# Kernel tuning notes

Hardware: AMD Instinct MI355X
Metric: run time of the kernel (lower is better)

## Reference

```python
import jax, jax.numpy as jnp
import numpy as np

LAMBDA_CONE = 0.5   # module-level constant in original repo
TAU_TEMP = 1.0      # softmax temperature
EPS = 1e-8


def setup_inputs() -> dict:
    key = jax.random.key(0)
    k1, k2, k3 = jax.random.split(key, 3)
    B, N, K, D = 8, 32768, 64, 64
    features = jax.random.normal(k1, (B, N, D), dtype=jnp.float32)
    slots = jax.random.normal(k2, (B, K, D), dtype=jnp.float32)
    horizons = jax.random.uniform(k3, (B, K), dtype=jnp.float32)  # positive horizons
    return {"features": features, "slots": slots, "horizons": horizons}


def _pairwise_minkowski(features, slots):
    # Minkowski split: channel 0 is time-like, channels 1: are space-like.
    ft, fs = features[..., 0], features[..., 1:]   # [B,N], [B,N,D-1]
    st, ss = slots[..., 0], slots[..., 1:]          # [B,K], [B,K,D-1]
    # dt[b,k,n] = t_feat - t_slot
    dt = ft[:, None, :] - st[:, :, None]            # [B,K,N]
    # squared spatial distance via the expansion ||f-s||^2 = ||f||^2 - 2 f.s + ||s||^2
    # (avoids materializing a [B,K,N,D] difference tensor)
    cross = jnp.einsum('bnd,bkd->bkn', fs, ss)      # [B,K,N]
    dx2 = (fs * fs).sum(-1)[:, None, :] - 2.0 * cross + (ss * ss).sum(-1)[:, :, None]
    dx2 = jnp.maximum(dx2, 0.0)                     # guard tiny negatives from expansion
    return dt, dx2


def reference(features, slots, horizons):
    dt, dx2 = _pairwise_minkowski(features, slots)  # [B,K,N] each
    # proper-time interval s^2 = dt^2 - |dx|^2; signed sqrt as the safe distance
    interval = dt * dt - dx2
    dist = jnp.sign(interval) * jnp.sqrt(jnp.abs(interval) + EPS)
    # cone score: how deep inside the light cone, scaled by per-slot horizon
    cone = (jnp.abs(dt) - jnp.sqrt(dx2 + EPS)) / (horizons[:, :, None] + EPS)
    logits = (-jnp.abs(dist) + jnp.tanh(cone) * LAMBDA_CONE) / TAU_TEMP
    attention = jax.nn.softmax(logits, axis=1)      # softmax over slots
    return attention
```

## Files before the change

kernel.cpp:

```cpp
#include <hip/hip_runtime.h>
#include <math.h>

#define EPSF 1e-8f

typedef _Float16 f16x8 __attribute__((ext_vector_type(8)));
typedef float    f32x4 __attribute__((ext_vector_type(4)));

constexpr int Bb = 8, Nn = 32768, Kk = 64, Dd = 64;

__global__ __launch_bounds__(256, 3) void attn_kernel(
    const float* __restrict__ features,
    const float* __restrict__ slots,
    const float* __restrict__ horizons,
    float* __restrict__ out)
{
    __shared__ float s_st[Kk], s_ss2[Kk], s_rh[Kk];

    const int tid  = threadIdx.x;
    const int bid  = blockIdx.x;
    const int b    = bid >> 7;
    const int blk  = bid & 127;
    const int lane = tid & 63;
    const int wid  = tid >> 6;
    const int m    = lane & 15;
    const int quad = lane >> 4;

    if (tid < Kk) {
        const float4* sr = (const float4*)(slots + (size_t)(b * Kk + tid) * Dd);
        float4 v = sr[0];
        float st = v.x;
        float ss = v.y * v.y + v.z * v.z + v.w * v.w;
        #pragma unroll
        for (int i = 1; i < 16; ++i) {
            float4 u = sr[i];
            ss += u.x * u.x + u.y * u.y + u.z * u.z + u.w * u.w;
        }
        s_st[tid]  = st;
        s_ss2[tid] = ss;
        s_rh[tid]  = 1.0f / (horizons[b * Kk + tid] + EPSF);
    }

    f16x8 a_hi[4][2], a_lo[4][2];
    #pragma unroll
    for (int t = 0; t < 4; ++t) {
        #pragma unroll
        for (int c = 0; c < 2; ++c) {
            const float* sp = slots + (size_t)(b * Kk + 16 * t + m) * Dd
                            + 32 * c + quad * 8;
            float4 u0 = *(const float4*)sp;
            float4 u1 = *(const float4*)(sp + 4);
            float fv[8] = {u0.x, u0.y, u0.z, u0.w, u1.x, u1.y, u1.z, u1.w};
            if (c == 0 && quad == 0) fv[0] = 0.0f;
            #pragma unroll
            for (int j = 0; j < 8; ++j) {
                float x = fv[j];
                _Float16 h = (_Float16)x;
                _Float16 l = (_Float16)(x - (float)h);
                a_hi[t][c][j] = h;
                a_lo[t][c][j] = l;
            }
        }
    }
    __syncthreads();

    #pragma unroll 1
    for (int it = 0; it < 4; ++it) {
        const int n0 = (blk * 16 + wid * 4 + it) * 16;

        f16x8 b_hi[2], b_lo[2];
        float f00 = 0.f, fs2p = 0.f;
        #pragma unroll
        for (int c = 0; c < 2; ++c) {
            const float* fp = features + (((size_t)b << 15) + n0 + m) * Dd
                            + 32 * c + quad * 8;
            float4 u0 = *(const float4*)fp;
            float4 u1 = *(const float4*)(fp + 4);
            float fv[8] = {u0.x, u0.y, u0.z, u0.w, u1.x, u1.y, u1.z, u1.w};
            if (c == 0) f00 = fv[0];
            #pragma unroll
            for (int j = 0; j < 8; ++j) {
                float x = fv[j];
                fs2p = fmaf(x, x, fs2p);
                _Float16 h = (_Float16)x;
                _Float16 l = (_Float16)(x - (float)h);
                b_hi[c][j] = h;
                b_lo[c][j] = l;
            }
        }
        const float ft = __shfl(f00, m);
        float fs2 = fs2p;
        fs2 += __shfl_xor(fs2, 16);
        fs2 += __shfl_xor(fs2, 32);
        fs2 = fmaf(-ft, ft, fs2);

        f32x4 acc[4];
        #pragma unroll
        for (int t = 0; t < 4; ++t) {
            f32x4 a = {0.f, 0.f, 0.f, 0.f};
            #pragma unroll
            for (int c = 0; c < 2; ++c) {
                a = __builtin_amdgcn_mfma_f32_16x16x32_f16(a_hi[t][c], b_hi[c], a, 0, 0, 0);
                a = __builtin_amdgcn_mfma_f32_16x16x32_f16(a_hi[t][c], b_lo[c], a, 0, 0, 0);
                a = __builtin_amdgcn_mfma_f32_16x16x32_f16(a_lo[t][c], b_hi[c], a, 0, 0, 0);
            }
            acc[t] = a;
        }

        float p[4][4];
        float sum = 0.f;
        #pragma unroll
        for (int t = 0; t < 4; ++t) {
            #pragma unroll
            for (int r = 0; r < 4; ++r) {
                const int k = 16 * t + quad * 4 + r;
                float st  = s_st[k];
                float ss2 = s_ss2[k];
                float rh  = s_rh[k];
                float cross = acc[t][r];
                float dt  = ft - st;
                float dx2 = fmaf(-2.f, cross, fs2 + ss2);
                dx2 = fmaxf(dx2, 0.f);
                float interval = fmaf(dt, dt, -dx2);
                float adist = __builtin_amdgcn_sqrtf(fabsf(interval) + EPSF);
                float cone  = (fabsf(dt) - __builtin_amdgcn_sqrtf(dx2 + EPSF)) * rh;
                float e  = __expf(2.0f * cone);
                float th = 1.0f - 2.0f * __builtin_amdgcn_rcpf(e + 1.0f);
                float logit = fmaf(0.5f, th, -adist);
                float pe = __expf(logit);
                p[t][r] = pe;
                sum += pe;
            }
        }
        sum += __shfl_xor(sum, 16);
        sum += __shfl_xor(sum, 32);
        const float inv = __builtin_amdgcn_rcpf(sum);

        float* ob = out + (((size_t)(b * Kk)) << 15) + n0 + m;
        #pragma unroll
        for (int t = 0; t < 4; ++t) {
            #pragma unroll
            for (int r = 0; r < 4; ++r) {
                const int k = 16 * t + quad * 4 + r;
                ob[(size_t)k << 15] = p[t][r] * inv;
            }
        }
    }
}

extern "C" void kernel_launch(void* const* d_in, const int* in_sizes, int n_in,
                              void* d_out, int out_size, void* d_ws, size_t ws_size,
                              hipStream_t stream) {
    const float* features = (const float*)d_in[0];
    const float* slots    = (const float*)d_in[1];
    const float* horizons = (const float*)d_in[2];
    float* out = (float*)d_out;

    hipLaunchKernelGGL(attn_kernel, dim3(1024), dim3(256), 0, stream,
                       features, slots, horizons, out);
}
```

Measured before the change: 144.8 us.

## Stage softmax outputs in LDS for float4 stores and prefetch next feature tile

Each wave now writes its unnormalized probabilities and per-column reciprocal sums into a padded LDS tile. Every two 16-column tiles it reads them back and emits 128-byte float4 row stores instead of scattered 64-byte scalar stores. Feature loads for the next tile are double-buffered in registers, and the launch bound hint goes from 3 to 4 blocks. This adds about 34KB of LDS per block and relies on 16-byte LDS reads at addresses whose row stride is padded to 33 floats, so some rows are not 16-byte aligned.

```diff
diff --git a/kernel.cpp b/kernel.cpp
--- a/kernel.cpp
+++ b/kernel.cpp
@@ -7,14 +7,17 @@
 typedef float    f32x4 __attribute__((ext_vector_type(4)));
 
 constexpr int Bb = 8, Nn = 32768, Kk = 64, Dd = 64;
+constexpr int PAD = 33;
 
-__global__ __launch_bounds__(256, 3) void attn_kernel(
+__global__ __launch_bounds__(256, 4) void attn_kernel(
     const float* __restrict__ features,
     const float* __restrict__ slots,
     const float* __restrict__ horizons,
     float* __restrict__ out)
 {
     __shared__ float s_st[Kk], s_ss2[Kk], s_rh[Kk];
+    __shared__ float s_p[4][Kk * PAD];
+    __shared__ float s_inv[4][32];
 
     const int tid  = threadIdx.x;
     const int bid  = blockIdx.x;
@@ -63,20 +66,39 @@
     }
     __syncthreads();
 
-    #pragma unroll 1
+    const int base_tile = blk * 16 + wid * 4;
+    float* const my_p   = s_p[wid];
+    float* const my_inv = s_inv[wid];
+
+    float4 buf[2][4];
+    {
+        const float* fp0 = features + (((size_t)b << 15) + (size_t)(base_tile) * 16 + m) * Dd
+                         + quad * 8;
+        buf[0][0] = *(const float4*)(fp0);
+        buf[0][1] = *(const float4*)(fp0 + 4);
+        buf[0][2] = *(const float4*)(fp0 + 32);
+        buf[0][3] = *(const float4*)(fp0 + 36);
+    }
+
+    #pragma unroll
     for (int it = 0; it < 4; ++it) {
-        const int n0 = (blk * 16 + wid * 4 + it) * 16;
+        if (it < 3) {
+            const float* fpn = features + (((size_t)b << 15) + (size_t)(base_tile + it + 1) * 16 + m) * Dd
+                             + quad * 8;
+            buf[(it + 1) & 1][0] = *(const float4*)(fpn);
+            buf[(it + 1) & 1][1] = *(const float4*)(fpn + 4);
+            buf[(it + 1) & 1][2] = *(const float4*)(fpn + 32);
+            buf[(it + 1) & 1][3] = *(const float4*)(fpn + 36);
+        }
 
         f16x8 b_hi[2], b_lo[2];
-        float f00 = 0.f, fs2p = 0.f;
+        const float f00 = buf[it & 1][0].x;
+        float fs2p = 0.f;
         #pragma unroll
         for (int c = 0; c < 2; ++c) {
-            const float* fp = features + (((size_t)b << 15) + n0 + m) * Dd
-                            + 32 * c + quad * 8;
-            float4 u0 = *(const float4*)fp;
-            float4 u1 = *(const float4*)(fp + 4);
+            float4 u0 = buf[it & 1][2 * c];
+            float4 u1 = buf[it & 1][2 * c + 1];
             float fv[8] = {u0.x, u0.y, u0.z, u0.w, u1.x, u1.y, u1.z, u1.w};
-            if (c == 0) f00 = fv[0];
             #pragma unroll
             for (int j = 0; j < 8; ++j) {
                 float x = fv[j];
@@ -106,7 +128,7 @@
             acc[t] = a;
         }
 
-        float p[4][4];
+        const int colb = (it & 1) * 16 + m;
         float sum = 0.f;
         #pragma unroll
         for (int t = 0; t < 4; ++t) {
@@ -127,22 +149,29 @@
                 float th = 1.0f - 2.0f * __builtin_amdgcn_rcpf(e + 1.0f);
                 float logit = fmaf(0.5f, th, -adist);
                 float pe = __expf(logit);
-                p[t][r] = pe;
+                my_p[k * PAD + colb] = pe;
                 sum += pe;
             }
         }
         sum += __shfl_xor(sum, 16);
         sum += __shfl_xor(sum, 32);
-        const float inv = __builtin_amdgcn_rcpf(sum);
+        my_inv[colb] = __builtin_amdgcn_rcpf(sum);
 
-        float* ob = out + (((size_t)(b * Kk)) << 15) + n0 + m;
-        #pragma unroll
-        for (int t = 0; t < 4; ++t) {
+        if (it & 1) {
+            asm volatile("s_waitcnt lgkmcnt(0)" ::: "memory");
+            const int r8 = lane >> 3;
+            const int c8 = lane & 7;
+            const size_t npair = (size_t)(base_tile + (it - 1)) * 16;
+            float4 iv = *(const float4*)(my_inv + c8 * 4);
+            float* ob = out + (((size_t)(b * Kk)) << 15) + npair + c8 * 4;
             #pragma unroll
-            for (int r = 0; r < 4; ++r) {
-                const int k = 16 * t + quad * 4 + r;
-                ob[(size_t)k << 15] = p[t][r] * inv;
+            for (int i = 0; i < 8; ++i) {
+                const int k = i * 8 + r8;
+                float4 v = *(const float4*)(my_p + k * PAD + c8 * 4);
+                v.x *= iv.x; v.y *= iv.y; v.z *= iv.z; v.w *= iv.w;
+                *(float4*)(ob + ((size_t)k << 15)) = v;
             }
+            asm volatile("s_waitcnt lgkmcnt(0)" ::: "memory");
         }
     }
 }
```

Result: slower. 170.9 us (+18.0%).

## Stage slot MFMA operands in LDS, prefetch features, double grid for occupancy

Applied to the files above, without the earlier changes.

The split-fp16 slot A-operands now live in shared memory. Each wave converts one 16-slot tile and all waves read them from LDS, where before every wave held all of them in registers. Register pressure drops, so launch bounds can rise to 4 blocks per CU. The grid doubles so each wave handles two 16-column tiles, with the second tile's feature loads issued before processing the first. The cost is extra LDS reads inside the MFMA loop and more blocks each redoing the slot preprocessing.

```diff
diff --git a/kernel.cpp b/kernel.cpp
--- a/kernel.cpp
+++ b/kernel.cpp
@@ -8,18 +8,20 @@
 
 constexpr int Bb = 8, Nn = 32768, Kk = 64, Dd = 64;
 
-__global__ __launch_bounds__(256, 3) void attn_kernel(
+__global__ __launch_bounds__(256, 4) void attn_kernel(
     const float* __restrict__ features,
     const float* __restrict__ slots,
     const float* __restrict__ horizons,
     float* __restrict__ out)
 {
     __shared__ float s_st[Kk], s_ss2[Kk], s_rh[Kk];
+    __shared__ f16x8 s_ahi[8][64];
+    __shared__ f16x8 s_alo[8][64];
 
     const int tid  = threadIdx.x;
     const int bid  = blockIdx.x;
-    const int b    = bid >> 7;
-    const int blk  = bid & 127;
+    const int b    = bid >> 8;
+    const int blk  = bid & 255;
     const int lane = tid & 63;
     const int wid  = tid >> 6;
     const int m    = lane & 15;
@@ -40,9 +42,8 @@
         s_rh[tid]  = 1.0f / (horizons[b * Kk + tid] + EPSF);
     }
 
-    f16x8 a_hi[4][2], a_lo[4][2];
-    #pragma unroll
-    for (int t = 0; t < 4; ++t) {
+    {
+        const int t = wid;
         #pragma unroll
         for (int c = 0; c < 2; ++c) {
             const float* sp = slots + (size_t)(b * Kk + 16 * t + m) * Dd
@@ -51,32 +52,53 @@
             float4 u1 = *(const float4*)(sp + 4);
             float fv[8] = {u0.x, u0.y, u0.z, u0.w, u1.x, u1.y, u1.z, u1.w};
             if (c == 0 && quad == 0) fv[0] = 0.0f;
+            f16x8 h8, l8;
             #pragma unroll
             for (int j = 0; j < 8; ++j) {
                 float x = fv[j];
                 _Float16 h = (_Float16)x;
                 _Float16 l = (_Float16)(x - (float)h);
-                a_hi[t][c][j] = h;
-                a_lo[t][c][j] = l;
+                h8[j] = h;
+                l8[j] = l;
             }
+            s_ahi[t * 2 + c][lane] = h8;
+            s_alo[t * 2 + c][lane] = l8;
         }
     }
     __syncthreads();
 
-    #pragma unroll 1
-    for (int it = 0; it < 4; ++it) {
-        const int n0 = (blk * 16 + wid * 4 + it) * 16;
+    const int base_tile = blk * 8 + wid * 2;
+
+    float4 buf[2][4];
+    {
+        const float* fp0 = features + (((size_t)b << 15) + (size_t)base_tile * 16 + m) * Dd
+                         + quad * 8;
+        buf[0][0] = *(const float4*)(fp0);
+        buf[0][1] = *(const float4*)(fp0 + 4);
+        buf[0][2] = *(const float4*)(fp0 + 32);
+        buf[0][3] = *(const float4*)(fp0 + 36);
+    }
+
+    #pragma unroll
+    for (int it = 0; it < 2; ++it) {
+        if (it == 0) {
+            const float* fpn = features + (((size_t)b << 15) + (size_t)(base_tile + 1) * 16 + m) * Dd
+                             + quad * 8;
+            buf[1][0] = *(const float4*)(fpn);
+            buf[1][1] = *(const float4*)(fpn + 4);
+            buf[1][2] = *(const float4*)(fpn + 32);
+            buf[1][3] = *(const float4*)(fpn + 36);
+        }
+        const int n0 = (base_tile + it) * 16;
 
         f16x8 b_hi[2], b_lo[2];
-        float f00 = 0.f, fs2p = 0.f;
+        const float f00 = buf[it][0].x;
+        float fs2p = 0.f;
         #pragma unroll
         for (int c = 0; c < 2; ++c) {
-            const float* fp = features + (((size_t)b << 15) + n0 + m) * Dd
-                            + 32 * c + quad * 8;
-            float4 u0 = *(const float4*)fp;
-            float4 u1 = *(const float4*)(fp + 4);
+            float4 u0 = buf[it][2 * c];
+            float4 u1 = buf[it][2 * c + 1];
             float fv[8] = {u0.x, u0.y, u0.z, u0.w, u1.x, u1.y, u1.z, u1.w};
-            if (c == 0) f00 = fv[0];
             #pragma unroll
             for (int j = 0; j < 8; ++j) {
                 float x = fv[j];
@@ -96,17 +118,20 @@
         f32x4 acc[4];
         #pragma unroll
         for (int t = 0; t < 4; ++t) {
+            f16x8 ah0 = s_ahi[t * 2 + 0][lane];
+            f16x8 ah1 = s_ahi[t * 2 + 1][lane];
+            f16x8 al0 = s_alo[t * 2 + 0][lane];
+            f16x8 al1 = s_alo[t * 2 + 1][lane];
             f32x4 a = {0.f, 0.f, 0.f, 0.f};
-            #pragma unroll
-            for (int c = 0; c < 2; ++c) {
-                a = __builtin_amdgcn_mfma_f32_16x16x32_f16(a_hi[t][c], b_hi[c], a, 0, 0, 0);
-                a = __builtin_amdgcn_mfma_f32_16x16x32_f16(a_hi[t][c], b_lo[c], a, 0, 0, 0);
-                a = __builtin_amdgcn_mfma_f32_16x16x32_f16(a_lo[t][c], b_hi[c], a, 0, 0, 0);
-            }
+            a = __builtin_amdgcn_mfma_f32_16x16x32_f16(ah0, b_hi[0], a, 0, 0, 0);
+            a = __builtin_amdgcn_mfma_f32_16x16x32_f16(ah0, b_lo[0], a, 0, 0, 0);
+            a = __builtin_amdgcn_mfma_f32_16x16x32_f16(al0, b_hi[0], a, 0, 0, 0);
+            a = __builtin_amdgcn_mfma_f32_16x16x32_f16(ah1, b_hi[1], a, 0, 0, 0);
+            a = __builtin_amdgcn_mfma_f32_16x16x32_f16(ah1, b_lo[1], a, 0, 0, 0);
+            a = __builtin_amdgcn_mfma_f32_16x16x32_f16(al1, b_hi[1], a, 0, 0, 0);
             acc[t] = a;
         }
 
-        float p[4][4];
         float sum = 0.f;
         #pragma unroll
         for (int t = 0; t < 4; ++t) {
@@ -127,7 +152,7 @@
                 float th = 1.0f - 2.0f * __builtin_amdgcn_rcpf(e + 1.0f);
                 float logit = fmaf(0.5f, th, -adist);
                 float pe = __expf(logit);
-                p[t][r] = pe;
+                acc[t][r] = pe;
                 sum += pe;
             }
         }
@@ -141,7 +166,7 @@
             #pragma unroll
             for (int r = 0; r < 4; ++r) {
                 const int k = 16 * t + quad * 4 + r;
-                ob[(size_t)k << 15] = p[t][r] * inv;
+                ob[(size_t)k << 15] = acc[t][r] * inv;
             }
         }
     }
@@ -155,6 +180,6 @@
     const float* horizons = (const float*)d_in[2];
     float* out = (float*)d_out;
 
-    hipLaunchKernelGGL(attn_kernel, dim3(1024), dim3(256), 0, stream,
+    hipLaunchKernelGGL(attn_kernel, dim3(2048), dim3(256), 0, stream,
                        features, slots, horizons, out);
 }
```

Result: faster. 127.2 us (-12.2%).
